# Kernel optimization log

Hardware: AMD Instinct MI355X
Metric: run time of the kernel (lower is better)

Reference implementation:

```python
import jax, jax.numpy as jnp
import numpy as np

B, N, P = 256, 12, 66
DN = 1024   # node_feature_size
DE = 1024   # edge_feature_size
D = 512     # message_size
DIMS = [3 * D, 1024, 512]  # shared trunk dims; heads differ only in out classes
C_LR, C_CR, C_MR = 9, 3, 5


def _mlp(x, Ws, bs):
    # ReLU MLP, no activation on final layer (eval mode: dropout is identity)
    for i, (W, b) in enumerate(zip(Ws, bs)):
        x = x @ W + b
        if i < len(Ws) - 1:
            x = jax.nn.relu(x)
    return x


def _head_params(key, out_dim):
    dims = DIMS + [out_dim]
    Ws, bs = [], []
    for i in range(len(dims) - 1):
        key, k = jax.random.split(key)
        Ws.append(jax.random.normal(k, (dims[i], dims[i + 1]), jnp.float32) * (1.0 / np.sqrt(dims[i])))
        bs.append(jnp.zeros((dims[i + 1],), jnp.float32))
    return Ws, bs


def setup_inputs() -> dict:
    key = jax.random.key(0)
    ks = jax.random.split(key, 12)
    inp = {
        'node_features': jax.random.normal(ks[0], (B, N, DN), jnp.float32),
        'edge_features': jax.random.normal(ks[1], (B, N, N, DE), jnp.float32),
        'edge_embeddings': jax.random.normal(ks[2], (B, N, N, D), jnp.float32),
        'pairs': jax.random.randint(ks[3], (B, P, 2), 0, N),
        'num_rels': jax.random.randint(ks[4], (B,), 0, P + 1),
        'W_node': jax.random.normal(ks[5], (DN, D), jnp.float32) * (1.0 / np.sqrt(DN)),
        'b_node': jnp.zeros((D,), jnp.float32),
        'W_edge': jax.random.normal(ks[6], (DE, D), jnp.float32) * (1.0 / np.sqrt(DE)),
        'b_edge': jnp.zeros((D,), jnp.float32),
    }
    for name, cdim, k in (('lr', C_LR, ks[7]), ('cr', C_CR, ks[8]), ('mr', C_MR, ks[9])):
        Ws, bs = _head_params(k, cdim)
        for i in range(3):
            inp[f'{name}_W{i}'] = Ws[i]
            inp[f'{name}_b{i}'] = bs[i]
    return inp


def reference(node_features, edge_features, edge_embeddings, pairs, num_rels,
              W_node, b_node, W_edge, b_edge,
              lr_W0, lr_b0, lr_W1, lr_b1, lr_W2, lr_b2,
              cr_W0, cr_b0, cr_W1, cr_b1, cr_W2, cr_b2,
              mr_W0, mr_b0, mr_W1, mr_b1, mr_W2, mr_b2):
    # feature resize linears
    nf = node_features @ W_node + b_node        # [B,N,D]
    ef = edge_features @ W_edge + b_edge        # [B,N,N,D]

    # vectorized make_classifier_inputs
    i0, i1 = pairs[..., 0], pairs[..., 1]       # [B,P]
    bidx = jnp.arange(nf.shape[0])[:, None]     # [B,1]
    n1 = nf[bidx, i0]                           # [B,P,D]
    n2 = nf[bidx, i1]                           # [B,P,D]
    emb_mean = 0.5 * (edge_embeddings[bidx, i0, i1] + edge_embeddings[bidx, i1, i0])
    feat_mean = 0.5 * (ef[bidx, i0, i1] + ef[bidx, i1, i0])
    e = 0.5 * (emb_mean + feat_mean)            # [B,P,D]
    ci = jnp.concatenate([n1, n2, e], axis=-1)  # [B,P,3D]

    # rows i >= num_rels[b] stay zero (preallocated-zeros semantics)
    valid = (jnp.arange(ci.shape[1])[None, :] < num_rels[:, None])[..., None]
    ci = jnp.where(valid, ci, jnp.zeros((), ci.dtype))

    lr = _mlp(ci, [lr_W0, lr_W1, lr_W2], [lr_b0, lr_b1, lr_b2])
    cr = _mlp(ci, [cr_W0, cr_W1, cr_W2], [cr_b0, cr_b1, cr_b2])
    mr = _mlp(ci, [mr_W0, mr_W1, mr_W2], [mr_b0, mr_b1, mr_b2])
    return lr, cr, mr
```

## Files before the change

### kernel.cpp

```cpp
#include <hip/hip_runtime.h>
#include <stdint.h>

#define BB 256
#define NNODE 12
#define PP 66
#define DNF 1024
#define DEF 1024
#define DD 512
#define MROWS (BB*PP)
#define MNODE (BB*NNODE)
#define MTILES (MROWS/128)

typedef __attribute__((ext_vector_type(8))) short s16x8;
typedef __attribute__((ext_vector_type(4))) float f32x4;
typedef __attribute__((ext_vector_type(8))) unsigned short u16x8;

__device__ __forceinline__ unsigned short f2bf(float f) {
  union { float f; unsigned u; } v; v.f = f;
  return (unsigned short)((v.u + 0x7FFFu + ((v.u >> 16) & 1u)) >> 16);
}
__device__ __forceinline__ float bf2f(unsigned short h) {
  union { unsigned u; float f; } v; v.u = ((unsigned)h) << 16;
  return v.f;
}

__device__ __forceinline__ void gll16(const void* g, void* l) {
  __builtin_amdgcn_global_load_lds(
      (const __attribute__((address_space(1))) void*)g,
      (__attribute__((address_space(3))) void*)l, 16, 0, 0);
}

__global__ __launch_bounds__(256) void k_scan_h1c(
    const int* __restrict__ nrels, int* __restrict__ offs,
    int* __restrict__ Mv, int2* __restrict__ nodes,
    const float* __restrict__ b0a, const float* __restrict__ b0b,
    const float* __restrict__ b0c,
    const float* __restrict__ W1a, const float* __restrict__ W1b,
    const float* __restrict__ W1c,
    float* __restrict__ h1part) {
  const int bid = blockIdx.x, t = threadIdx.x;
  if (bid == 24) {
    __shared__ int s[256];
    const int val = nrels[t];
    s[t] = val;
    __syncthreads();
    for (int d = 1; d < 256; d <<= 1) {
      int x = (t >= d) ? s[t - d] : 0;
      __syncthreads();
      s[t] += x;
      __syncthreads();
    }
    offs[t] = s[t] - val;
    __syncthreads();
    const int total = s[255];
    if (t == 0) *Mv = total;
    if (t < 128) {
      int cr = total + t;
      if (cr < MROWS) nodes[cr] = make_int2(0, 0);
    }
    return;
  }
  const int h = bid >> 3, c = bid & 7;
  const float* b0 = h == 0 ? b0a : (h == 1 ? b0b : b0c);
  const float* W1 = h == 0 ? W1a : (h == 1 ? W1b : W1c);
  const int k0 = c * 128;
  float acc0 = 0.f, acc1 = 0.f;
#pragma unroll 8
  for (int kk = 0; kk < 128; ++kk) {
    const int k = k0 + kk;
    const float bv = fmaxf(b0[k], 0.f);
    acc0 += bv * W1[(size_t)k * 512 + t];
    acc1 += bv * W1[(size_t)k * 512 + t + 256];
  }
  h1part[(size_t)bid * 512 + t] = acc0;
  h1part[(size_t)bid * 512 + t + 256] = acc1;
}

__global__ __launch_bounds__(512) void k_finish(
    const float* __restrict__ h1part,
    const float* __restrict__ b1a, const float* __restrict__ b1b,
    const float* __restrict__ b1c,
    const float* __restrict__ w2a, const float* __restrict__ w2b,
    const float* __restrict__ w2c,
    const float* __restrict__ b2a, const float* __restrict__ b2b,
    const float* __restrict__ b2c, float* __restrict__ outc) {
  const int t = threadIdx.x;
  __shared__ float red[9];
  for (int h = 0; h < 3; ++h) {
    const float* b1 = h == 0 ? b1a : (h == 1 ? b1b : b1c);
    const float* W2 = h == 0 ? w2a : (h == 1 ? w2b : w2c);
    const float* b2 = h == 0 ? b2a : (h == 1 ? b2b : b2c);
    const int C = h == 0 ? 9 : (h == 1 ? 3 : 5);
    const int obase = h == 0 ? 0 : (h == 1 ? 9 : 12);
    if (t < 9) red[t] = 0.f;
    float s = b1[t];
#pragma unroll
    for (int cc = 0; cc < 8; ++cc)
      s += h1part[(size_t)(h * 8 + cc) * 512 + t];
    const float hv = fmaxf(s, 0.f);
    __syncthreads();
    float p[9] = {0.f, 0.f, 0.f, 0.f, 0.f, 0.f, 0.f, 0.f, 0.f};
#pragma unroll
    for (int c = 0; c < 9; ++c)
      if (c < C) p[c] = hv * W2[(size_t)t * C + c];
#pragma unroll
    for (int c = 0; c < 9; ++c)
#pragma unroll
      for (int off = 32; off; off >>= 1) p[c] += __shfl_xor(p[c], off);
    if ((t & 63) == 0)
      for (int c = 0; c < C; ++c) atomicAdd(&red[c], p[c]);
    __syncthreads();
    if (t < C) outc[obase + t] = red[t] + b2[t];
    __syncthreads();
  }
}

__global__ __launch_bounds__(256) void k_fillout(const float* __restrict__ outc,
                                                 float* __restrict__ out) {
  const int e = blockIdx.x * 256 + threadIdx.x;
  if (e >= MROWS * 17) return;
  int c;
  if (e < MROWS * 9) c = e % 9;
  else if (e < MROWS * 12) c = 9 + (e - MROWS * 9) % 3;
  else c = 12 + (e - MROWS * 12) % 5;
  out[e] = outc[c];
}

__global__ __launch_bounds__(256) void k_prep(
    const float* __restrict__ node, unsigned short* __restrict__ node_bf,
    const float* __restrict__ W_node, unsigned short* __restrict__ WnT,
    const float* __restrict__ W_edge, unsigned short* __restrict__ WeT,
    const float* __restrict__ W0a, const float* __restrict__ W0b,
    const float* __restrict__ W0c, unsigned short* __restrict__ W0T,
    const float* __restrict__ W1a, const float* __restrict__ W1b,
    const float* __restrict__ W1c, unsigned short* __restrict__ W1T,
    const float* __restrict__ w2a, const float* __restrict__ w2b,
    const float* __restrict__ w2c,
    const float* __restrict__ b2a, const float* __restrict__ b2b,
    const float* __restrict__ b2c,
    unsigned short* __restrict__ W2T, float* __restrict__ b2pad,
    const float* __restrict__ b0a, const float* __restrict__ b0b,
    const float* __restrict__ b0c, float* __restrict__ b0cat,
    const float* __restrict__ b1a, const float* __restrict__ b1b,
    const float* __restrict__ b1c, float* __restrict__ b1cat,
    const float* __restrict__ b_node, const float* __restrict__ b_edge,
    float* __restrict__ b_ne) {
  __shared__ float tile[64][65];
  const int bid = blockIdx.x, t = threadIdx.x;
  if (bid < 3072) {
    int i = bid * 256 + t;
    float4 v = ((const float4*)node)[i];
    ushort4 o;
    o.x = f2bf(v.x); o.y = f2bf(v.y); o.z = f2bf(v.z); o.w = f2bf(v.w);
    ((ushort4*)node_bf)[i] = o;
  } else if (bid < 4864) {
    int tau = bid - 3072;
    const float* src; unsigned short* dst; int K, N;
    if (tau < 128)       { src = W_node; dst = WnT; K = 1024; N = 512; }
    else if (tau < 256)  { src = W_edge; dst = WeT; K = 1024; N = 512; tau -= 128; }
    else if (tau < 1408) {
      int hh = (tau - 256) / 384; tau = (tau - 256) % 384;
      src = hh == 0 ? W0a : (hh == 1 ? W0b : W0c);
      dst = W0T + (size_t)hh * 1024 * 1536; K = 1536; N = 1024;
    } else {
      int hh = (tau - 1408) / 128; tau = (tau - 1408) % 128;
      src = hh == 0 ? W1a : (hh == 1 ? W1b : W1c);
      dst = W1T + (size_t)hh * 512 * 1024; K = 1024; N = 512;
    }
    const int ntn = N >> 6;
    const int kb = (tau / ntn) * 64, nb = (tau % ntn) * 64;
    const int tx = t & 15, ty = t >> 4;
#pragma unroll
    for (int i = 0; i < 4; i++) {
      float4 v = *(const float4*)&src[(size_t)(kb + ty + 16 * i) * N + nb + tx * 4];
      tile[ty + 16 * i][tx * 4 + 0] = v.x;
      tile[ty + 16 * i][tx * 4 + 1] = v.y;
      tile[ty + 16 * i][tx * 4 + 2] = v.z;
      tile[ty + 16 * i][tx * 4 + 3] = v.w;
    }
    __syncthreads();
    const int wx = t & 7, wy = t >> 3;
#pragma unroll
    for (int i = 0; i < 2; i++) {
      const int n = wy + 32 * i;
      u16x8 o;
#pragma unroll
      for (int j = 0; j < 8; j++) o[j] = f2bf(tile[wx * 8 + j][n]);
      *(u16x8*)&dst[(size_t)(nb + n) * K + kb + wx * 8] = o;
    }
  } else if (bid < 5632) {
    int e = bid - 4864;
    int h = e >> 8, blk = e & 255;
    const int C = (h == 0) ? 9 : ((h == 1) ? 3 : 5);
    const float* W2 = (h == 0) ? w2a : ((h == 1) ? w2b : w2c);
    const float* b2 = (h == 0) ? b2a : ((h == 1) ? b2b : b2c);
    int idx = blk * 256 + t;
    int n = idx >> 9, k = idx & 511;
    W2T[(size_t)h * 65536 + idx] = (n < C) ? f2bf(W2[(size_t)k * C + n]) : (unsigned short)0;
    if (blk == 0 && t < 128)
      b2pad[h * 128 + t] = (t < C) ? b2[t] : 0.f;
  } else if (bid < 5644) {
    int j = bid - 5632;
    const float* b0 = (j < 4) ? b0a : (j < 8 ? b0b : b0c);
    b0cat[j * 256 + t] = b0[(j & 3) * 256 + t];
  } else if (bid < 5650) {
    int j = bid - 5644;
    const float* b1 = (j < 2) ? b1a : (j < 4 ? b1b : b1c);
    b1cat[j * 256 + t] = b1[(j & 1) * 256 + t];
  } else {
    int idx = (bid - 5650) * 256 + t;
    b_ne[idx] = (idx < 512) ? b_node[idx] : b_edge[idx - 512];
  }
}

__global__ __launch_bounds__(256) void k_gather_ef(const float* __restrict__ EF,
                                                   const float* __restrict__ EE,
                                                   const int* __restrict__ pairs,
                                                   const int* __restrict__ nrels,
                                                   const int* __restrict__ offs,
                                                   unsigned short* __restrict__ efm,
                                                   unsigned short* __restrict__ emb,
                                                   int2* __restrict__ nodes,
                                                   int* __restrict__ rmap) {
  int r = blockIdx.x;
  int b = r / PP, p = r - b * PP;
  if (p >= nrels[b]) return;
  const int cr = offs[b] + p;
  int i0 = pairs[r * 2 + 0], i1 = pairs[r * 2 + 1];
  int t = threadIdx.x;
  if (t == 0) {
    nodes[cr] = make_int2(b * NNODE + i0, b * NNODE + i1);
    rmap[cr] = r;
  }
  const float4* e01 = (const float4*)(EF + ((size_t)((b * NNODE + i0) * NNODE + i1)) * DEF);
  const float4* e10 = (const float4*)(EF + ((size_t)((b * NNODE + i1) * NNODE + i0)) * DEF);
  float4 a = e01[t], c = e10[t];
  ushort4 o;
  o.x = f2bf(0.5f * (a.x + c.x));
  o.y = f2bf(0.5f * (a.y + c.y));
  o.z = f2bf(0.5f * (a.z + c.z));
  o.w = f2bf(0.5f * (a.w + c.w));
  ((ushort4*)(efm + (size_t)cr * DEF))[t] = o;
  const float2* g01 = (const float2*)(EE + ((size_t)((b * NNODE + i0) * NNODE + i1)) * DD);
  const float2* g10 = (const float2*)(EE + ((size_t)((b * NNODE + i1) * NNODE + i0)) * DD);
  float2 x = g01[t], y = g10[t];
  ushort2 eo;
  eo.x = f2bf(0.25f * (x.x + y.x));
  eo.y = f2bf(0.25f * (x.y + y.y));
  ((ushort2*)(emb + (size_t)cr * DD))[t] = eo;
}

template <int EPI>
__global__ __launch_bounds__(256) void k_gemm(
    const unsigned short* __restrict__ A, int ldA,
    const unsigned short* __restrict__ BT, int ldB, int K,
    int Ntiles,
    const float* __restrict__ bias,
    unsigned short* __restrict__ outb, int ldo,
    const unsigned short* __restrict__ em,
    const int* __restrict__ Mvp,
    unsigned short* __restrict__ ci,
    int blocksPerHead, long long aHeadOff, long long bHeadOff,
    long long oHeadOff, int biasHeadOff,
    const int2* __restrict__ nodes,
    const unsigned short* __restrict__ nfa,
    const unsigned short* __restrict__ nfb,
    const int* __restrict__ rmap) {
  __shared__ __align__(16) unsigned short sm[16896];
  char* smc = (char*)sm;
  const int t = threadIdx.x;
  const int l = t & 63, w = t >> 6;
  const int wm = w >> 1, wn = w & 1;
  int bid = blockIdx.x;

  int head = 0;
  unsigned short* outp = outb;
  if constexpr (EPI == 3) {
    head = bid / MTILES;
    bid -= head * MTILES;
    A += (size_t)head * MROWS * DD;
    BT += (size_t)head * 128 * DD;
    bias += head * 128;
  } else {
    if (blocksPerHead > 0) {
      head = bid / blocksPerHead;
      bid -= head * blocksPerHead;
      A += (long long)head * aHeadOff;
      BT += (long long)head * bHeadOff;
      bias += head * biasHeadOff;
      outp = outb + (long long)head * oHeadOff;
    }
  }
  const int tn = bid % Ntiles, tm = bid / Ntiles;

  int Mv = MROWS;
  if (Mvp) Mv = *Mvp;
  if constexpr (EPI == 6) { if (head == 0) Mv = MNODE; }
  if (Mvp) {
    if (tm * 128 >= Mv) return;
  }

  const int lrow = l >> 3;
  const int scol = (l & 7) ^ lrow;
  const unsigned short* Ap = A + (size_t)(tm * 128 + w * 8 + lrow) * ldA + scol * 8;
  const unsigned short* Bp = BT + (size_t)(tn * 128 + w * 8 + lrow) * ldB + scol * 8;

  f32x4 acc[4][4] = {};
  const int hi = l >> 4, l15 = l & 15, l7 = l & 7;
  const int nk = K >> 6;

  for (int kt = 0; kt < nk; ++kt) {
#pragma unroll
    for (int c = 0; c < 4; ++c) {
      gll16(Ap + (size_t)c * 32 * ldA, smc + c * 4096 + w * 1024);
      gll16(Bp + (size_t)c * 32 * ldB, smc + 16384 + c * 4096 + w * 1024);
    }
    __syncthreads();
#pragma unroll
    for (int kk = 0; kk < 2; ++kk) {
      const int cb = (((kk << 2) + hi) ^ l7) << 4;
      s16x8 af[4], bfr[4];
#pragma unroll
      for (int m = 0; m < 4; m++)
        af[m] = *(const s16x8*)(smc + (wm * 64 + m * 16 + l15) * 128 + cb);
#pragma unroll
      for (int n = 0; n < 4; n++)
        bfr[n] = *(const s16x8*)(smc + 16384 + (wn * 64 + n * 16 + l15) * 128 + cb);
#pragma unroll
      for (int m = 0; m < 4; m++)
#pragma unroll
        for (int n = 0; n < 4; n++)
          asm volatile("v_mfma_f32_16x16x32_bf16 %0, %1, %2, %0"
                       : "+v"(acc[m][n])
                       : "v"(af[m]), "v"(bfr[n]));
    }
    __syncthreads();
    Ap += 64;
    Bp += 64;
  }
  asm volatile("s_nop 7\n\ts_nop 7\n\ts_nop 7" :::);

  if constexpr (EPI == 5) {
    const int se_r = t >> 4;
    const int se_c = (t & 15) * 8;
#pragma unroll
    for (int it = 0; it < 8; ++it) {
      const int rr = se_r + (it << 4);
      const int2 nn = nodes[tm * 128 + rr];
      union { unsigned short s[8]; unsigned long long q[2]; } ov;
      u16x8 va = *(const u16x8*)&nfa[(size_t)nn.x * 3072 + tn * 128 + se_c];
      u16x8 vb = *(const u16x8*)&nfb[(size_t)nn.y * 3072 + tn * 128 + se_c];
#pragma unroll
      for (int j = 0; j < 8; ++j)
        ov.s[j] = f2bf(bf2f(va[j]) + bf2f(vb[j]));
      *(unsigned long long*)(smc + rr * 264 + se_c * 2) = ov.q[0];
      *(unsigned long long*)(smc + rr * 264 + se_c * 2 + 8) = ov.q[1];
    }
    __syncthreads();
  }

  const int gr_base = tm * 128 + wm * 64 + (hi << 2);
  const int gc_base = tn * 128 + wn * 64 + l15;
  const int lr_base = wm * 64 + (hi << 2);
  const int lc_base = wn * 64 + l15;

  int Cc = 0; size_t obase = 0;
  if constexpr (EPI == 3) {
    Cc = (head == 0) ? 9 : ((head == 1) ? 3 : 5);
    obase = (head == 0) ? 0 : ((head == 1) ? (size_t)MROWS * 9 : (size_t)MROWS * 12);
  }

#pragma unroll
  for (int n = 0; n < 4; n++) {
    const int gc = gc_base + n * 16;
    const float bv = (EPI == 4) ? 0.f : bias[gc];
#pragma unroll
    for (int m = 0; m < 4; m++) {
#pragma unroll
      for (int i = 0; i < 4; i++) {
        const int gr = gr_base + m * 16 + i;
        float v = acc[m][n][i] + bv;
        if constexpr (EPI == 0 || EPI == 4) {
          outp[(size_t)gr * ldo + gc] = f2bf(v);
        } else if constexpr (EPI == 2) {
          outp[(size_t)gr * ldo + gc] = f2bf(v > 0.f ? v : 0.f);
        } else if constexpr (EPI == 5) {
          const int lr = lr_base + m * 16 + i;
          const int lc = lc_base + n * 16;
          v += bf2f(*(const unsigned short*)(smc + lr * 264 + lc * 2));
          outp[(size_t)gr * ldo + gc] = f2bf(v > 0.f ? v : 0.f);
        } else if constexpr (EPI == 6) {
          if (head == 0) {
            outp[(size_t)gr * ldo + gc] = f2bf(v);
          } else {
            float e = bf2f(em[(size_t)gr * DD + gc]) + 0.5f * v;
            ci[(size_t)gr * DD + gc] = f2bf(e);
          }
        } else {
          if (gc < Cc && gr < Mv)
            ((float*)outb)[obase + (size_t)rmap[gr] * Cc + gc] = v;
        }
      }
    }
  }
}

extern "C" void kernel_launch(void* const* d_in, const int* in_sizes, int n_in,
                              void* d_out, int out_size, void* d_ws, size_t ws_size,
                              hipStream_t stream) {
  const float* node   = (const float*)d_in[0];
  const float* EF     = (const float*)d_in[1];
  const float* EE     = (const float*)d_in[2];
  const int*   pairs  = (const int*)d_in[3];
  const int*   nrels  = (const int*)d_in[4];
  const float* W_node = (const float*)d_in[5];
  const float* b_node = (const float*)d_in[6];
  const float* W_edge = (const float*)d_in[7];
  const float* b_edge = (const float*)d_in[8];
  const float* hW0[3] = {(const float*)d_in[9],  (const float*)d_in[15], (const float*)d_in[21]};
  const float* hb0[3] = {(const float*)d_in[10], (const float*)d_in[16], (const float*)d_in[22]};
  const float* hW1[3] = {(const float*)d_in[11], (const float*)d_in[17], (const float*)d_in[23]};
  const float* hb1[3] = {(const float*)d_in[12], (const float*)d_in[18], (const float*)d_in[24]};
  const float* hW2[3] = {(const float*)d_in[13], (const float*)d_in[19], (const float*)d_in[25]};
  const float* hb2[3] = {(const float*)d_in[14], (const float*)d_in[20], (const float*)d_in[26]};

  char* ws = (char*)d_ws;
  size_t off = 0;
  auto alloc = [&](size_t bytes) {
    char* p = ws + off;
    off += (bytes + 255) & ~(size_t)255;
    return p;
  };
  unsigned short* WnT    = (unsigned short*)alloc((size_t)512 * 1024 * 2);
  unsigned short* WeT    = (unsigned short*)alloc((size_t)512 * 1024 * 2);
  unsigned short* W0T    = (unsigned short*)alloc((size_t)3072 * 1536 * 2);
  unsigned short* W1T    = (unsigned short*)alloc((size_t)3 * 512 * 1024 * 2);
  unsigned short* W2T    = (unsigned short*)alloc((size_t)3 * 128 * 512 * 2);
  float*          b2pad  = (float*)alloc((size_t)3 * 128 * 4);
  float*          b0cat  = (float*)alloc((size_t)3072 * 4);
  float*          b1cat  = (float*)alloc((size_t)1536 * 4);
  float*          b_ne   = (float*)alloc((size_t)1024 * 4);
  int2*           nodes  = (int2*)alloc((size_t)MROWS * 8);
  int*            offs   = (int*)alloc((size_t)256 * 4);
  int*            Mv     = (int*)alloc(256);
  int*            rmap   = (int*)alloc((size_t)MROWS * 4);
  float*          outc   = (float*)alloc((size_t)32 * 4);
  float*          h1part = (float*)alloc((size_t)24 * 512 * 4);
  size_t zoneA = off;
  unsigned short* efm = (unsigned short*)alloc((size_t)MROWS * DEF * 2);
  unsigned short* EMb = (unsigned short*)alloc((size_t)MROWS * DD * 2);
  unsigned short* ci_e = (unsigned short*)alloc((size_t)MROWS * DD * 2);
  size_t zoneC = off;
  unsigned short* node_bf = (unsigned short*)alloc((size_t)MNODE * DNF * 2);
  unsigned short* nf      = (unsigned short*)alloc((size_t)MNODE * DD * 2);
  unsigned short* nfa   = (unsigned short*)(ws + zoneA);
  unsigned short* nfb   = nfa + (size_t)MNODE * 3072;
  unsigned short* h1    = (unsigned short*)(ws + zoneA);
  unsigned short* h0big = (unsigned short*)(ws + zoneC);

  k_scan_h1c<<<25, 256, 0, stream>>>(nrels, offs, Mv, nodes,
      hb0[0], hb0[1], hb0[2], hW1[0], hW1[1], hW1[2], h1part);
  k_finish<<<1, 512, 0, stream>>>(h1part, hb1[0], hb1[1], hb1[2],
      hW2[0], hW2[1], hW2[2], hb2[0], hb2[1], hb2[2], outc);
  k_prep<<<5654, 256, 0, stream>>>(node, node_bf, W_node, WnT, W_edge, WeT,
      hW0[0], hW0[1], hW0[2], W0T, hW1[0], hW1[1], hW1[2], W1T,
      hW2[0], hW2[1], hW2[2], hb2[0], hb2[1], hb2[2], W2T, b2pad,
      hb0[0], hb0[1], hb0[2], b0cat, hb1[0], hb1[1], hb1[2], b1cat,
      b_node, b_edge, b_ne);
  k_fillout<<<(MROWS * 17 + 255) / 256, 256, 0, stream>>>(outc, (float*)d_out);
  k_gather_ef<<<MROWS, 256, 0, stream>>>(EF, EE, pairs, nrels, offs,
                                         efm, EMb, nodes, rmap);

  k_gemm<6><<<2 * MTILES * 4, 256, 0, stream>>>(
      node_bf, 1024, WnT, 1024, 1024, 4, b_ne, nf, 512,
      EMb, Mv, ci_e, MTILES * 4,
      (long long)(efm - node_bf), (long long)512 * 1024,
      (long long)(ci_e - nf), 512,
      nullptr, nullptr, nullptr, nullptr);

  k_gemm<4><<<2 * (MNODE / 128) * 24, 256, 0, stream>>>(
      nf, 512, W0T, 1536, 512, 24, nullptr, nfa, 3072,
      nullptr, nullptr, nullptr, (MNODE / 128) * 24,
      0, 512, (long long)MNODE * 3072, 0, nullptr, nullptr, nullptr, nullptr);

  k_gemm<5><<<MTILES * 24, 256, 0, stream>>>(
      ci_e, 512, W0T + 1024, 1536, 512, 24, b0cat, h0big, 3072,
      nullptr, Mv, nullptr, 0, 0, 0, 0, 0, nodes, nfa, nfb, nullptr);

  k_gemm<2><<<3 * MTILES * 4, 256, 0, stream>>>(
      h0big, 3072, W1T, 1024, 1024, 4, b1cat, h1, 512,
      nullptr, Mv, nullptr, MTILES * 4,
      1024, (long long)512 * 1024, (long long)MROWS * DD, 512,
      nullptr, nullptr, nullptr, nullptr);

  k_gemm<3><<<3 * MTILES, 256, 0, stream>>>(
      h1, 512, W2T, 512, 512, 1, b2pad, (unsigned short*)d_out, 0,
      nullptr, Mv, nullptr, 0, 0, 0, 0, 0, nullptr, nullptr, nullptr, rmap);
}
```

Before: 213.0 us.

## Merge prep, fill-out and edge gather into one launch; swizzle epilogue smem

```diff
diff --git a/kernel.cpp b/kernel.cpp
--- a/kernel.cpp
+++ b/kernel.cpp
@@ -115,18 +115,7 @@
   }
 }
 
-__global__ __launch_bounds__(256) void k_fillout(const float* __restrict__ outc,
-                                                 float* __restrict__ out) {
-  const int e = blockIdx.x * 256 + threadIdx.x;
-  if (e >= MROWS * 17) return;
-  int c;
-  if (e < MROWS * 9) c = e % 9;
-  else if (e < MROWS * 12) c = 9 + (e - MROWS * 9) % 3;
-  else c = 12 + (e - MROWS * 12) % 5;
-  out[e] = outc[c];
-}
-
-__global__ __launch_bounds__(256) void k_prep(
+__global__ __launch_bounds__(256) void k_prep_all(
     const float* __restrict__ node, unsigned short* __restrict__ node_bf,
     const float* __restrict__ W_node, unsigned short* __restrict__ WnT,
     const float* __restrict__ W_edge, unsigned short* __restrict__ WeT,
@@ -144,7 +133,13 @@
     const float* __restrict__ b1a, const float* __restrict__ b1b,
     const float* __restrict__ b1c, float* __restrict__ b1cat,
     const float* __restrict__ b_node, const float* __restrict__ b_edge,
-    float* __restrict__ b_ne) {
+    float* __restrict__ b_ne,
+    const float* __restrict__ EF, const float* __restrict__ EE,
+    const int* __restrict__ pairs, const int* __restrict__ nrels,
+    const int* __restrict__ offs,
+    unsigned short* __restrict__ efm, unsigned short* __restrict__ emb,
+    int2* __restrict__ nodes, int* __restrict__ rmap,
+    const float* __restrict__ outc, float* __restrict__ out) {
   __shared__ float tile[64][65];
   const int bid = blockIdx.x, t = threadIdx.x;
   if (bid < 3072) {
@@ -207,47 +202,44 @@
     int j = bid - 5644;
     const float* b1 = (j < 2) ? b1a : (j < 4 ? b1b : b1c);
     b1cat[j * 256 + t] = b1[(j & 1) * 256 + t];
-  } else {
+  } else if (bid < 5654) {
     int idx = (bid - 5650) * 256 + t;
     b_ne[idx] = (idx < 512) ? b_node[idx] : b_edge[idx - 512];
-  }
-}
-
-__global__ __launch_bounds__(256) void k_gather_ef(const float* __restrict__ EF,
-                                                   const float* __restrict__ EE,
-                                                   const int* __restrict__ pairs,
-                                                   const int* __restrict__ nrels,
-                                                   const int* __restrict__ offs,
-                                                   unsigned short* __restrict__ efm,
-                                                   unsigned short* __restrict__ emb,
-                                                   int2* __restrict__ nodes,
-                                                   int* __restrict__ rmap) {
-  int r = blockIdx.x;
-  int b = r / PP, p = r - b * PP;
-  if (p >= nrels[b]) return;
-  const int cr = offs[b] + p;
-  int i0 = pairs[r * 2 + 0], i1 = pairs[r * 2 + 1];
-  int t = threadIdx.x;
-  if (t == 0) {
-    nodes[cr] = make_int2(b * NNODE + i0, b * NNODE + i1);
-    rmap[cr] = r;
-  }
-  const float4* e01 = (const float4*)(EF + ((size_t)((b * NNODE + i0) * NNODE + i1)) * DEF);
-  const float4* e10 = (const float4*)(EF + ((size_t)((b * NNODE + i1) * NNODE + i0)) * DEF);
-  float4 a = e01[t], c = e10[t];
-  ushort4 o;
-  o.x = f2bf(0.5f * (a.x + c.x));
-  o.y = f2bf(0.5f * (a.y + c.y));
-  o.z = f2bf(0.5f * (a.z + c.z));
-  o.w = f2bf(0.5f * (a.w + c.w));
-  ((ushort4*)(efm + (size_t)cr * DEF))[t] = o;
-  const float2* g01 = (const float2*)(EE + ((size_t)((b * NNODE + i0) * NNODE + i1)) * DD);
-  const float2* g10 = (const float2*)(EE + ((size_t)((b * NNODE + i1) * NNODE + i0)) * DD);
-  float2 x = g01[t], y = g10[t];
-  ushort2 eo;
-  eo.x = f2bf(0.25f * (x.x + y.x));
-  eo.y = f2bf(0.25f * (x.y + y.y));
-  ((ushort2*)(emb + (size_t)cr * DD))[t] = eo;
+  } else if (bid < 22550) {
+    int r = bid - 5654;
+    int b = r / PP, p = r - b * PP;
+    if (p >= nrels[b]) return;
+    const int cr = offs[b] + p;
+    int i0 = pairs[r * 2 + 0], i1 = pairs[r * 2 + 1];
+    if (t == 0) {
+      nodes[cr] = make_int2(b * NNODE + i0, b * NNODE + i1);
+      rmap[cr] = r;
+    }
+    const float4* e01 = (const float4*)(EF + ((size_t)((b * NNODE + i0) * NNODE + i1)) * DEF);
+    const float4* e10 = (const float4*)(EF + ((size_t)((b * NNODE + i1) * NNODE + i0)) * DEF);
+    float4 a = e01[t], c = e10[t];
+    ushort4 o;
+    o.x = f2bf(0.5f * (a.x + c.x));
+    o.y = f2bf(0.5f * (a.y + c.y));
+    o.z = f2bf(0.5f * (a.z + c.z));
+    o.w = f2bf(0.5f * (a.w + c.w));
+    ((ushort4*)(efm + (size_t)cr * DEF))[t] = o;
+    const float2* g01 = (const float2*)(EE + ((size_t)((b * NNODE + i0) * NNODE + i1)) * DD);
+    const float2* g10 = (const float2*)(EE + ((size_t)((b * NNODE + i1) * NNODE + i0)) * DD);
+    float2 x = g01[t], y = g10[t];
+    ushort2 eo;
+    eo.x = f2bf(0.25f * (x.x + y.x));
+    eo.y = f2bf(0.25f * (x.y + y.y));
+    ((ushort2*)(emb + (size_t)cr * DD))[t] = eo;
+  } else {
+    const int e = (bid - 22550) * 256 + t;
+    if (e >= MROWS * 17) return;
+    int c;
+    if (e < MROWS * 9) c = e % 9;
+    else if (e < MROWS * 12) c = 9 + (e - MROWS * 9) % 3;
+    else c = 12 + (e - MROWS * 12) % 5;
+    out[e] = outc[c];
+  }
 }
 
 template <int EPI>
@@ -266,7 +258,7 @@
     const unsigned short* __restrict__ nfa,
     const unsigned short* __restrict__ nfb,
     const int* __restrict__ rmap) {
-  __shared__ __align__(16) unsigned short sm[16896];
+  __shared__ __align__(16) unsigned short sm[16384];
   char* smc = (char*)sm;
   const int t = threadIdx.x;
   const int l = t & 63, w = t >> 6;
@@ -342,19 +334,20 @@
 
   if constexpr (EPI == 5) {
     const int se_r = t >> 4;
-    const int se_c = (t & 15) * 8;
+    const int se_ch = t & 15;
 #pragma unroll
     for (int it = 0; it < 8; ++it) {
       const int rr = se_r + (it << 4);
       const int2 nn = nodes[tm * 128 + rr];
       union { unsigned short s[8]; unsigned long long q[2]; } ov;
-      u16x8 va = *(const u16x8*)&nfa[(size_t)nn.x * 3072 + tn * 128 + se_c];
-      u16x8 vb = *(const u16x8*)&nfb[(size_t)nn.y * 3072 + tn * 128 + se_c];
+      u16x8 va = *(const u16x8*)&nfa[(size_t)nn.x * 3072 + tn * 128 + se_ch * 8];
+      u16x8 vb = *(const u16x8*)&nfb[(size_t)nn.y * 3072 + tn * 128 + se_ch * 8];
 #pragma unroll
       for (int j = 0; j < 8; ++j)
         ov.s[j] = f2bf(bf2f(va[j]) + bf2f(vb[j]));
-      *(unsigned long long*)(smc + rr * 264 + se_c * 2) = ov.q[0];
-      *(unsigned long long*)(smc + rr * 264 + se_c * 2 + 8) = ov.q[1];
+      const int sch = se_ch ^ ((rr >> 2) & 7);
+      *(unsigned long long*)(smc + rr * 256 + (sch << 4)) = ov.q[0];
+      *(unsigned long long*)(smc + rr * 256 + (sch << 4) + 8) = ov.q[1];
     }
     __syncthreads();
   }
@@ -387,7 +380,8 @@
         } else if constexpr (EPI == 5) {
           const int lr = lr_base + m * 16 + i;
           const int lc = lc_base + n * 16;
-          v += bf2f(*(const unsigned short*)(smc + lr * 264 + lc * 2));
+          const int rch = (lc >> 3) ^ ((lr >> 2) & 7);
+          v += bf2f(*(const unsigned short*)(smc + lr * 256 + (rch << 4) + (lc & 7) * 2));
           outp[(size_t)gr * ldo + gc] = f2bf(v > 0.f ? v : 0.f);
         } else if constexpr (EPI == 6) {
           if (head == 0) {
@@ -462,14 +456,13 @@
       hb0[0], hb0[1], hb0[2], hW1[0], hW1[1], hW1[2], h1part);
   k_finish<<<1, 512, 0, stream>>>(h1part, hb1[0], hb1[1], hb1[2],
       hW2[0], hW2[1], hW2[2], hb2[0], hb2[1], hb2[2], outc);
-  k_prep<<<5654, 256, 0, stream>>>(node, node_bf, W_node, WnT, W_edge, WeT,
+  k_prep_all<<<23672, 256, 0, stream>>>(node, node_bf, W_node, WnT, W_edge, WeT,
       hW0[0], hW0[1], hW0[2], W0T, hW1[0], hW1[1], hW1[2], W1T,
       hW2[0], hW2[1], hW2[2], hb2[0], hb2[1], hb2[2], W2T, b2pad,
       hb0[0], hb0[1], hb0[2], b0cat, hb1[0], hb1[1], hb1[2], b1cat,
-      b_node, b_edge, b_ne);
-  k_fillout<<<(MROWS * 17 + 255) / 256, 256, 0, stream>>>(outc, (float*)d_out);
-  k_gather_ef<<<MROWS, 256, 0, stream>>>(EF, EE, pairs, nrels, offs,
-                                         efm, EMb, nodes, rmap);
+      b_node, b_edge, b_ne,
+      EF, EE, pairs, nrels, offs, efm, EMb, nodes, rmap,
+      outc, (float*)d_out);
 
   k_gemm<6><<<2 * MTILES * 4, 256, 0, stream>>>(
       node_bf, 1024, WnT, 1024, 1024, 4, b_ne, nf, 512,
```

Measured after the change: 208.6 us. 1.02x faster.
